# Performance work log

Hardware: AMD Instinct MI355X
Metric: run time of the kernel (lower is better)

Reference implementation:

```python
import jax, jax.numpy as jnp
import numpy as np

MIN_WIN = 40.0   # cfg.MIN_WINDOW_SIZE (frames)
MAX_WIN = 200.0  # cfg.MAX_WINDOW_SIZE (frames)
NUM_ANCHORS = 10 # num_anchors_per_frame
NUM_CLASS = 2    # output_dim


def setup_inputs() -> dict:
    key = jax.random.key(0)
    k0, k1, k2 = jax.random.split(key, 3)
    B, T, D = 64, 4096, 256
    A, C = NUM_ANCHORS, NUM_CLASS
    x = jax.random.normal(k0, (B, T, D), dtype=jnp.float32)
    W_cls = jax.random.normal(k1, (A * C, D), dtype=jnp.float32) * 0.02
    b_cls = jnp.zeros((A * C,), dtype=jnp.float32)
    W_bbox = jax.random.normal(k2, (A * 2, D), dtype=jnp.float32) * 0.02
    b_bbox = jnp.zeros((A * 2,), dtype=jnp.float32)
    return {"x": x, "W_cls": W_cls, "b_cls": b_cls, "W_bbox": W_bbox, "b_bbox": b_bbox}


def _make_anchors(T):
    # one anchor per (frame, window-size): centered at frame t with length L
    centers = jnp.arange(T, dtype=jnp.float32)                              # [T]
    lengths = jnp.linspace(MIN_WIN, MAX_WIN, NUM_ANCHORS, dtype=jnp.float32)  # [A]
    start = centers[:, None] - (lengths[None, :] - 1.0) * 0.5               # [T, A]
    end = centers[:, None] + (lengths[None, :] - 1.0) * 0.5                 # [T, A]
    return jnp.stack([start.reshape(-1), end.reshape(-1)], axis=-1)         # [T*A, 2]


def reference(x, W_cls, b_cls, W_bbox, b_bbox):
    B, T, D = x.shape
    A, C = NUM_ANCHORS, NUM_CLASS
    # dual linear heads
    rpn_cls_score = (jnp.einsum('btd,od->bto', x, W_cls) + b_cls).reshape(B, T * A, C)
    rpn_bbox_pred = (jnp.einsum('btd,od->bto', x, W_bbox) + b_bbox).reshape(B, T * A, 2)
    # proposal layer: decode (dx, dl) deltas against anchors, clip to utterance
    anchors_per_utt = _make_anchors(T)                    # [T*A, 2]
    a_len = anchors_per_utt[:, 1] - anchors_per_utt[:, 0] + 1.0
    a_ctr = anchors_per_utt[:, 0] + 0.5 * (a_len - 1.0)
    dx = rpn_bbox_pred[..., 0]                            # [B, T*A]
    dl = rpn_bbox_pred[..., 1]
    p_ctr = dx * a_len + a_ctr
    p_len = jnp.exp(dl) * a_len
    start = jnp.clip(p_ctr - 0.5 * (p_len - 1.0), 0.0, T - 1.0)
    end = jnp.clip(p_ctr + 0.5 * (p_len - 1.0), 0.0, T - 1.0)
    proposals = jnp.stack([start, end], axis=-1)          # [B, T*A, 2]
    return anchors_per_utt, proposals, rpn_cls_score, rpn_bbox_pred
```

## Files before the change

### kernel.cpp

```cpp
#include <hip/hip_runtime.h>
#include <hip/hip_bf16.h>

constexpr int Bb = 64;
constexpr int T  = 4096;
constexpr int D  = 256;
constexpr int A  = 10;
constexpr size_t ANCHORS_N  = (size_t)T * A * 2;
constexpr size_t PER_TENSOR = (size_t)Bb * T * A * 2;
constexpr int M      = Bb * T;
constexpr int MT     = M / 16;
constexpr int NBLK   = 512;
constexpr int NWAVES = NBLK * 2;
constexpr int TPW    = MT / NWAVES;

typedef __attribute__((ext_vector_type(8))) short short8v;
typedef __attribute__((ext_vector_type(4))) float f32x4;

__device__ __forceinline__ unsigned short f2b(float f) {
    return __builtin_bit_cast(unsigned short, __float2bfloat16(f));
}
__device__ __forceinline__ float b2f(unsigned short h) {
    return __builtin_bit_cast(float, (unsigned)h << 16);
}

__global__ __launch_bounds__(128, 1) void rpn_mfma(
    const float* __restrict__ x,
    const float* __restrict__ Wc, const float* __restrict__ bc,
    const float* __restrict__ Wb, const float* __restrict__ bb,
    float* __restrict__ out_anch, float* __restrict__ out_prop,
    float* __restrict__ out_cls,  float* __restrict__ out_bbox)
{
    __shared__ float xs[2][2][16 * 256];

    const int tid  = threadIdx.x;
    const int w    = tid >> 6;
    const int lane = tid & 63;
    const int wid  = blockIdx.x * 2 + w;
    const int c    = lane & 15;
    const int kc   = lane >> 4;
    const int r3   = c & 7;

    float* const lb0 = &xs[w][0][0];
    float* const lb1 = &xs[w][1][0];

    auto stage = [&](float* lbuf, int mt) {
        const float* gbase = x + (size_t)mt * (16 * D);
#pragma unroll
        for (int r = 0; r < 16; ++r) {
            const float* g = gbase + r * D + ((lane ^ (r & 7)) << 2);
            __builtin_amdgcn_global_load_lds(
                (const __attribute__((address_space(1))) unsigned int*)g,
                (__attribute__((address_space(3))) unsigned int*)(lbuf + r * 256),
                16, 0, 0);
        }
    };

    stage(lb0, wid);
    {
        const int i = wid * 64 + lane;
        if (i < T * A) {
            const int t = i / A;
            const int a = i - t * A;
            const float L = fmaf((float)a, 160.0f / 9.0f, 40.0f);
            const float h = 0.5f * (L - 1.0f);
            reinterpret_cast<float2*>(out_anch)[i] = make_float2((float)t - h, (float)t + h);
        }
    }

    const float* wrow[3];
    float bias[3];
    bool  pad[3];
    wrow[0] = Wc + c * D;            bias[0] = bc[c];      pad[0] = false;
    if (c < 4) { wrow[1] = Wc + (16 + c) * D; bias[1] = bc[16 + c]; }
    else       { wrow[1] = Wb + (c - 4) * D;  bias[1] = bb[c - 4];  }
    pad[1] = false;
    if (c < 8) { wrow[2] = Wb + (12 + c) * D; bias[2] = bb[12 + c]; pad[2] = false; }
    else       { wrow[2] = Wb;                bias[2] = 0.0f;       pad[2] = true;  }

    short8v wf[3][8];
#pragma unroll
    for (int nt = 0; nt < 3; ++nt) {
#pragma unroll
        for (int ks = 0; ks < 8; ++ks) {
            const float* p = wrow[nt] + kc * 8 + ks * 32;
            const float4 a = *reinterpret_cast<const float4*>(p);
            const float4 b = *reinterpret_cast<const float4*>(p + 4);
            short8v h;
            h[0] = (short)f2b(a.x); h[1] = (short)f2b(a.y);
            h[2] = (short)f2b(a.z); h[3] = (short)f2b(a.w);
            h[4] = (short)f2b(b.x); h[5] = (short)f2b(b.y);
            h[6] = (short)f2b(b.z); h[7] = (short)f2b(b.w);
            if (pad[nt]) {
#pragma unroll
                for (int e = 0; e < 8; ++e) h[e] = 0;
            }
            wf[nt][ks] = h;
        }
    }

    const int offA = (((2 * kc) ^ r3) << 2);
    const int offB = (((2 * kc + 1) ^ r3) << 2);

    auto compute = [&](const float* lbuf, int mt) {
        const float* lrow = lbuf + c * 256;

        f32x4 ah0 = {0,0,0,0}, ah1 = {0,0,0,0}, ah2 = {0,0,0,0};
        f32x4 al0 = {0,0,0,0}, al1 = {0,0,0,0}, al2 = {0,0,0,0};

#pragma unroll
        for (int ks = 0; ks < 8; ++ks) {
            const float4 qa = *reinterpret_cast<const float4*>(lrow + ks * 32 + offA);
            const float4 qb = *reinterpret_cast<const float4*>(lrow + ks * 32 + offB);
            float v[8] = {qa.x, qa.y, qa.z, qa.w, qb.x, qb.y, qb.z, qb.w};
            short8v xh, xl;
#pragma unroll
            for (int e = 0; e < 8; ++e) {
                const unsigned short hb = f2b(v[e]);
                xh[e] = (short)hb;
                xl[e] = (short)f2b(v[e] - b2f(hb));
            }
            ah0 = __builtin_amdgcn_mfma_f32_16x16x32_bf16(xh, wf[0][ks], ah0, 0, 0, 0);
            al0 = __builtin_amdgcn_mfma_f32_16x16x32_bf16(xl, wf[0][ks], al0, 0, 0, 0);
            ah1 = __builtin_amdgcn_mfma_f32_16x16x32_bf16(xh, wf[1][ks], ah1, 0, 0, 0);
            al1 = __builtin_amdgcn_mfma_f32_16x16x32_bf16(xl, wf[1][ks], al1, 0, 0, 0);
            ah2 = __builtin_amdgcn_mfma_f32_16x16x32_bf16(xh, wf[2][ks], ah2, 0, 0, 0);
            al2 = __builtin_amdgcn_mfma_f32_16x16x32_bf16(xl, wf[2][ks], al2, 0, 0, 0);
        }

#pragma unroll
        for (int r = 0; r < 4; ++r) {
            const int    R  = mt * 16 + kc * 4 + r;
            const size_t rb = (size_t)R * 20;

            const float v0 = ah0[r] + al0[r] + bias[0];
            out_cls[rb + c] = v0;

            const float v1  = ah1[r] + al1[r] + bias[1];
            const float v1p = __shfl_xor(v1, 1);
            const float v2  = ah2[r] + al2[r] + bias[2];
            const float v2p = __shfl_xor(v2, 1);

            const int t = R & (T - 1);

            if (c < 4) {
                out_cls[rb + 16 + c] = v1;
            } else {
                const int jb = c - 4;
                out_bbox[rb + jb] = v1;
                if (!(jb & 1)) {
                    const int   an = jb >> 1;
                    const float L  = fmaf((float)an, 160.0f / 9.0f, 40.0f);
                    const float ctr = fmaf(v1, L, (float)t);
                    const float pl  = __expf(v1p) * L;
                    const float hh  = 0.5f * (pl - 1.0f);
                    const float s = fminf(fmaxf(ctr - hh, 0.0f), (float)(T - 1));
                    const float e = fminf(fmaxf(ctr + hh, 0.0f), (float)(T - 1));
                    *reinterpret_cast<float2*>(out_prop + rb + jb) = make_float2(s, e);
                }
            }
            if (c < 8) {
                const int jb = 12 + c;
                out_bbox[rb + jb] = v2;
                if (!(jb & 1)) {
                    const int   an = jb >> 1;
                    const float L  = fmaf((float)an, 160.0f / 9.0f, 40.0f);
                    const float ctr = fmaf(v2, L, (float)t);
                    const float pl  = __expf(v2p) * L;
                    const float hh  = 0.5f * (pl - 1.0f);
                    const float s = fminf(fmaxf(ctr - hh, 0.0f), (float)(T - 1));
                    const float e = fminf(fmaxf(ctr + hh, 0.0f), (float)(T - 1));
                    *reinterpret_cast<float2*>(out_prop + rb + jb) = make_float2(s, e);
                }
            }
        }
    };

    asm volatile("s_waitcnt vmcnt(0)" ::: "memory");
    __builtin_amdgcn_sched_barrier(0);

#pragma unroll 1
    for (int i = 0; i < TPW; ++i) {
        float* const cur = (i & 1) ? lb1 : lb0;
        float* const nxt = (i & 1) ? lb0 : lb1;
        if (i + 1 < TPW) stage(nxt, wid + (i + 1) * NWAVES);
        compute(cur, wid + i * NWAVES);
        asm volatile("s_waitcnt vmcnt(0)" ::: "memory");
        __builtin_amdgcn_sched_barrier(0);
    }
}

extern "C" void kernel_launch(void* const* d_in, const int* in_sizes, int n_in,
                              void* d_out, int out_size, void* d_ws, size_t ws_size,
                              hipStream_t stream) {
    const float* x  = (const float*)d_in[0];
    const float* Wc = (const float*)d_in[1];
    const float* bc = (const float*)d_in[2];
    const float* Wb = (const float*)d_in[3];
    const float* bb = (const float*)d_in[4];

    float* out     = (float*)d_out;
    float* anchors = out;
    float* prop    = out + ANCHORS_N;
    float* cls     = out + ANCHORS_N + PER_TENSOR;
    float* bbox    = out + ANCHORS_N + 2 * PER_TENSOR;

    rpn_mfma<<<NBLK, 128, 0, stream>>>(x, Wc, bc, Wb, bb, anchors, prop, cls, bbox);
}
```

Baseline: 73.64 us.

## Drop bf16 split-precision pass and pipeline x tiles in half-K chunks with 4 waves

Removes the low-part bf16 correction MFMAs, so x is rounded once to bf16 and only three MFMAs run per k-step instead of six. The per-wave LDS buffers are reorganised into two half-K (128-column) chunks that are refilled independently, which lets the load of the next tile overlap the compute and epilogue of the current one. The block size doubles to 256 threads with two blocks per CU, giving more waves to hide memory latency. The cost is reduced accuracy, since products now use single-bf16 x, which could exceed tolerance, and the vmcnt-based waits are more intricate.

Result: slower. 80.68 us (+9.6%).

```diff
diff --git a/kernel.cpp b/kernel.cpp
--- a/kernel.cpp
+++ b/kernel.cpp
@@ -10,7 +10,7 @@
 constexpr int M      = Bb * T;
 constexpr int MT     = M / 16;
 constexpr int NBLK   = 512;
-constexpr int NWAVES = NBLK * 2;
+constexpr int NWAVES = NBLK * 4;
 constexpr int TPW    = MT / NWAVES;
 
 typedef __attribute__((ext_vector_type(8))) short short8v;
@@ -19,63 +19,55 @@
 __device__ __forceinline__ unsigned short f2b(float f) {
     return __builtin_bit_cast(unsigned short, __float2bfloat16(f));
 }
-__device__ __forceinline__ float b2f(unsigned short h) {
-    return __builtin_bit_cast(float, (unsigned)h << 16);
-}
-
-__global__ __launch_bounds__(128, 1) void rpn_mfma(
+
+__global__ __launch_bounds__(256, 2) void rpn_mfma(
     const float* __restrict__ x,
     const float* __restrict__ Wc, const float* __restrict__ bc,
     const float* __restrict__ Wb, const float* __restrict__ bb,
     float* __restrict__ out_anch, float* __restrict__ out_prop,
     float* __restrict__ out_cls,  float* __restrict__ out_bbox)
 {
-    __shared__ float xs[2][2][16 * 256];
+    __shared__ float xs[4][2][16 * 128];
 
     const int tid  = threadIdx.x;
     const int w    = tid >> 6;
     const int lane = tid & 63;
-    const int wid  = blockIdx.x * 2 + w;
+    const int wid  = blockIdx.x * 4 + w;
     const int c    = lane & 15;
     const int kc   = lane >> 4;
-    const int r3   = c & 7;
 
     float* const lb0 = &xs[w][0][0];
     float* const lb1 = &xs[w][1][0];
 
-    auto stage = [&](float* lbuf, int mt) {
-        const float* gbase = x + (size_t)mt * (16 * D);
-#pragma unroll
-        for (int r = 0; r < 16; ++r) {
-            const float* g = gbase + r * D + ((lane ^ (r & 7)) << 2);
+    int goff[8];
+    {
+        const int hi5 = lane >> 5, ch = lane & 31;
+#pragma unroll
+        for (int i = 0; i < 8; ++i) {
+            const int r = 2 * i + hi5;
+            goff[i] = r * D + ((ch ^ (r & 7)) << 2);
+        }
+    }
+
+    auto stage = [&](float* lbuf, int mt, int h) {
+        const float* gb = x + (size_t)mt * (16 * D) + h * 128;
+#pragma unroll
+        for (int i = 0; i < 8; ++i) {
             __builtin_amdgcn_global_load_lds(
-                (const __attribute__((address_space(1))) unsigned int*)g,
-                (__attribute__((address_space(3))) unsigned int*)(lbuf + r * 256),
+                (const __attribute__((address_space(1))) unsigned int*)(gb + goff[i]),
+                (__attribute__((address_space(3))) unsigned int*)(lbuf + i * 256),
                 16, 0, 0);
         }
     };
 
-    stage(lb0, wid);
-    {
-        const int i = wid * 64 + lane;
-        if (i < T * A) {
-            const int t = i / A;
-            const int a = i - t * A;
-            const float L = fmaf((float)a, 160.0f / 9.0f, 40.0f);
-            const float h = 0.5f * (L - 1.0f);
-            reinterpret_cast<float2*>(out_anch)[i] = make_float2((float)t - h, (float)t + h);
-        }
-    }
-
     const float* wrow[3];
-    float bias[3];
-    bool  pad[3];
-    wrow[0] = Wc + c * D;            bias[0] = bc[c];      pad[0] = false;
-    if (c < 4) { wrow[1] = Wc + (16 + c) * D; bias[1] = bc[16 + c]; }
-    else       { wrow[1] = Wb + (c - 4) * D;  bias[1] = bb[c - 4];  }
-    pad[1] = false;
-    if (c < 8) { wrow[2] = Wb + (12 + c) * D; bias[2] = bb[12 + c]; pad[2] = false; }
-    else       { wrow[2] = Wb;                bias[2] = 0.0f;       pad[2] = true;  }
+    float bias0, bias1, bias2;
+    bool  pad2;
+    wrow[0] = Wc + c * D;                       bias0 = bc[c];
+    wrow[1] = (c < 4) ? Wc + (16 + c) * D : Wb + (c - 4) * D;
+    bias1   = (c < 4) ? bc[16 + c] : bb[c - 4];
+    if (c < 8) { wrow[2] = Wb + (12 + c) * D; bias2 = bb[12 + c]; pad2 = false; }
+    else       { wrow[2] = Wb;                bias2 = 0.0f;       pad2 = true;  }
 
     short8v wf[3][8];
 #pragma unroll
@@ -90,54 +82,61 @@
             h[2] = (short)f2b(a.z); h[3] = (short)f2b(a.w);
             h[4] = (short)f2b(b.x); h[5] = (short)f2b(b.y);
             h[6] = (short)f2b(b.z); h[7] = (short)f2b(b.w);
-            if (pad[nt]) {
+            if (nt == 2 && pad2) {
 #pragma unroll
                 for (int e = 0; e < 8; ++e) h[e] = 0;
             }
             wf[nt][ks] = h;
         }
     }
-
-    const int offA = (((2 * kc) ^ r3) << 2);
-    const int offB = (((2 * kc + 1) ^ r3) << 2);
-
-    auto compute = [&](const float* lbuf, int mt) {
-        const float* lrow = lbuf + c * 256;
-
-        f32x4 ah0 = {0,0,0,0}, ah1 = {0,0,0,0}, ah2 = {0,0,0,0};
-        f32x4 al0 = {0,0,0,0}, al1 = {0,0,0,0}, al2 = {0,0,0,0};
-
-#pragma unroll
-        for (int ks = 0; ks < 8; ++ks) {
-            const float4 qa = *reinterpret_cast<const float4*>(lrow + ks * 32 + offA);
-            const float4 qb = *reinterpret_cast<const float4*>(lrow + ks * 32 + offB);
-            float v[8] = {qa.x, qa.y, qa.z, qa.w, qb.x, qb.y, qb.z, qb.w};
-            short8v xh, xl;
-#pragma unroll
-            for (int e = 0; e < 8; ++e) {
-                const unsigned short hb = f2b(v[e]);
-                xh[e] = (short)hb;
-                xl[e] = (short)f2b(v[e] - b2f(hb));
-            }
-            ah0 = __builtin_amdgcn_mfma_f32_16x16x32_bf16(xh, wf[0][ks], ah0, 0, 0, 0);
-            al0 = __builtin_amdgcn_mfma_f32_16x16x32_bf16(xl, wf[0][ks], al0, 0, 0, 0);
-            ah1 = __builtin_amdgcn_mfma_f32_16x16x32_bf16(xh, wf[1][ks], ah1, 0, 0, 0);
-            al1 = __builtin_amdgcn_mfma_f32_16x16x32_bf16(xl, wf[1][ks], al1, 0, 0, 0);
-            ah2 = __builtin_amdgcn_mfma_f32_16x16x32_bf16(xh, wf[2][ks], ah2, 0, 0, 0);
-            al2 = __builtin_amdgcn_mfma_f32_16x16x32_bf16(xl, wf[2][ks], al2, 0, 0, 0);
-        }
-
+    asm volatile("" : "+v"(bias0), "+v"(bias1), "+v"(bias2));
+
+    {
+        const int i = wid * 64 + lane;
+        if (i < T * A) {
+            const int t = i / A;
+            const int a = i - t * A;
+            const float L = fmaf((float)a, 160.0f / 9.0f, 40.0f);
+            const float h = 0.5f * (L - 1.0f);
+            reinterpret_cast<float2*>(out_anch)[i] = make_float2((float)t - h, (float)t + h);
+        }
+    }
+
+    stage(lb0, wid, 0);
+    stage(lb1, wid, 1);
+
+    const int sw = (c & 7);
+
+    auto compute_half = [&](const float* lbuf, int h, f32x4& a0, f32x4& a1, f32x4& a2) {
+        const float* lrow = lbuf + c * 128;
+#pragma unroll
+        for (int ks = 0; ks < 4; ++ks) {
+            const int ch0 = ks * 8 + kc * 2;
+            const float4 qa = *reinterpret_cast<const float4*>(lrow + ((ch0 ^ sw) << 2));
+            const float4 qb = *reinterpret_cast<const float4*>(lrow + (((ch0 + 1) ^ sw) << 2));
+            const float v[8] = {qa.x, qa.y, qa.z, qa.w, qb.x, qb.y, qb.z, qb.w};
+            short8v xh;
+#pragma unroll
+            for (int e = 0; e < 8; ++e) xh[e] = (short)f2b(v[e]);
+            const int ksg = h * 4 + ks;
+            a0 = __builtin_amdgcn_mfma_f32_16x16x32_bf16(xh, wf[0][ksg], a0, 0, 0, 0);
+            a1 = __builtin_amdgcn_mfma_f32_16x16x32_bf16(xh, wf[1][ksg], a1, 0, 0, 0);
+            a2 = __builtin_amdgcn_mfma_f32_16x16x32_bf16(xh, wf[2][ksg], a2, 0, 0, 0);
+        }
+    };
+
+    auto epilogue = [&](int mt, const f32x4& a0, const f32x4& a1, const f32x4& a2) {
 #pragma unroll
         for (int r = 0; r < 4; ++r) {
             const int    R  = mt * 16 + kc * 4 + r;
             const size_t rb = (size_t)R * 20;
 
-            const float v0 = ah0[r] + al0[r] + bias[0];
+            const float v0 = a0[r] + bias0;
             out_cls[rb + c] = v0;
 
-            const float v1  = ah1[r] + al1[r] + bias[1];
+            const float v1  = a1[r] + bias1;
             const float v1p = __shfl_xor(v1, 1);
-            const float v2  = ah2[r] + al2[r] + bias[2];
+            const float v2  = a2[r] + bias2;
             const float v2p = __shfl_xor(v2, 1);
 
             const int t = R & (T - 1);
@@ -175,17 +174,23 @@
         }
     };
 
-    asm volatile("s_waitcnt vmcnt(0)" ::: "memory");
-    __builtin_amdgcn_sched_barrier(0);
-
 #pragma unroll 1
-    for (int i = 0; i < TPW; ++i) {
-        float* const cur = (i & 1) ? lb1 : lb0;
-        float* const nxt = (i & 1) ? lb0 : lb1;
-        if (i + 1 < TPW) stage(nxt, wid + (i + 1) * NWAVES);
-        compute(cur, wid + i * NWAVES);
-        asm volatile("s_waitcnt vmcnt(0)" ::: "memory");
+    for (int t = 0; t < TPW; ++t) {
+        const int mt = wid + t * NWAVES;
+        f32x4 a0 = {0,0,0,0}, a1 = {0,0,0,0}, a2 = {0,0,0,0};
+
+        asm volatile("s_waitcnt vmcnt(8)" ::: "memory");
         __builtin_amdgcn_sched_barrier(0);
+        compute_half(lb0, 0, a0, a1, a2);
+        if (t + 1 < TPW) stage(lb0, wid + (t + 1) * NWAVES, 0);
+
+        if (t + 1 < TPW) { asm volatile("s_waitcnt vmcnt(8)" ::: "memory"); }
+        else             { asm volatile("s_waitcnt vmcnt(0)" ::: "memory"); }
+        __builtin_amdgcn_sched_barrier(0);
+        compute_half(lb1, 1, a0, a1, a2);
+
+        epilogue(mt, a0, a1, a2);
+        if (t + 1 < TPW) stage(lb1, wid + (t + 1) * NWAVES, 1);
     }
 }
 
@@ -204,5 +209,5 @@
     float* cls     = out + ANCHORS_N + PER_TENSOR;
     float* bbox    = out + ANCHORS_N + 2 * PER_TENSOR;
 
-    rpn_mfma<<<NBLK, 128, 0, stream>>>(x, Wc, bc, Wb, bb, anchors, prop, cls, bbox);
+    rpn_mfma<<<NBLK, 256, 0, stream>>>(x, Wc, bc, Wb, bb, anchors, prop, cls, bbox);
 }
```
